# Performance work log

Hardware: AMD Instinct MI355X
Metric: run time of the kernel (lower is better)

## Reference

```python
import jax, jax.numpy as jnp
import numpy as np
import math

B, S, D, H = 2, 2048, 512, 8
HD = D // H

def setup_inputs() -> dict:
    key = jax.random.key(0)
    ks = jax.random.split(key, 13)
    scale = 1.0 / math.sqrt(D)
    inp = {
        "q_in": jax.random.normal(ks[0], (B, S, D), jnp.float32),
        "k_in": jax.random.normal(ks[1], (B, S, D), jnp.float32),
        "v_in": jax.random.normal(ks[2], (B, S, D), jnp.float32),
        "mask": jax.random.randint(ks[3], (B, 1, S, S), 0, 2, jnp.int32),
        "W1": jax.random.uniform(ks[4], (D, D), jnp.float32, -scale, scale),
        "b1": jax.random.uniform(ks[5], (D,), jnp.float32, -scale, scale),
        "W2": jax.random.uniform(ks[6], (D, D), jnp.float32, -scale, scale),
        "b2": jax.random.uniform(ks[7], (D,), jnp.float32, -scale, scale),
        "W3": jax.random.uniform(ks[8], (D, D), jnp.float32, -scale, scale),
        "b3": jax.random.uniform(ks[9], (D,), jnp.float32, -scale, scale),
        "Wo": jax.random.uniform(ks[10], (D, D), jnp.float32, -scale, scale),
        "bo": jax.random.uniform(ks[11], (D,), jnp.float32, -scale, scale),
    }
    return inp

def reference(q_in, k_in, v_in, mask, W1, b1, W2, b2, W3, b3, Wo, bo):
    # Linear projections (torch Linear: y = x @ W.T + b)
    q = q_in @ W1.T + b1  # [B,S,D]
    k = k_in @ W2.T + b2
    v = v_in @ W3.T + b3
    # split heads -> [B,H,S,HD]
    def split(x):
        return x.reshape(B, S, H, HD).transpose(0, 2, 1, 3)
    q, k, v = split(q), split(k), split(v)
    scores = jnp.einsum("bhqd,bhkd->bhqk", q, k) / math.sqrt(HD)
    scores = jnp.where(mask == 0, jnp.float32(-1e9), scores)
    attn = jax.nn.softmax(scores, axis=-1)
    out = jnp.einsum("bhqk,bhkd->bhqd", attn, v)  # [B,H,S,HD]
    out = out.transpose(0, 2, 1, 3).reshape(B, S, D)
    return out @ Wo.T + bo
```

## Files before the change

kernel.cpp:

```cpp
#include <hip/hip_runtime.h>
#include <hip/hip_bf16.h>
#include <math.h>

constexpr int B_ = 2, S_ = 2048, D_ = 512, H_ = 8, HD_ = 64;
constexpr int M_ = B_ * S_;
constexpr int NT_ = S_ / 64;
constexpr int NSPLIT = 2;
constexpr int NT2 = NT_ / NSPLIT;
constexpr int ROWS = B_ * S_ * H_;
constexpr int NGROUPS = (B_ * S_ * NT_) / 4;

typedef short s16x8 __attribute__((ext_vector_type(8)));
typedef float f32x4 __attribute__((ext_vector_type(4)));
typedef unsigned short u16;
typedef unsigned long long u64;

#define SWZ(b) ((b) ^ ((((b) >> 7) & 7) << 4))

constexpr float SCL = 0.18033688f;

static __device__ __forceinline__ unsigned int cvt_pk2(float lo, float hi) {
  __hip_bfloat162 h = __float22bfloat162_rn(make_float2(lo, hi));
  return *(unsigned int*)&h;
}
static __device__ __forceinline__ u16 cvt1(float f) {
  __hip_bfloat16 h = __float2bfloat16(f);
  return *(u16*)&h;
}
static __device__ __forceinline__ uint4 pack8(float4 a, float4 b) {
  uint4 r;
  r.x = cvt_pk2(a.x, a.y); r.y = cvt_pk2(a.z, a.w);
  r.z = cvt_pk2(b.x, b.y); r.w = cvt_pk2(b.z, b.w);
  return r;
}
static __device__ __forceinline__ float4 sum_scale(float4 a, float4 b, float s) {
  return make_float4((a.x + b.x) * s, (a.y + b.y) * s,
                     (a.z + b.z) * s, (a.w + b.w) * s);
}

#define QKV_STEP(BUF, T)                                                      \
  {                                                                           \
    const bool more_ = ((T) < 7);                                             \
    if (more_) {                                                              \
      const int o4 = ((T) + 1) * 16;                                          \
      fx[0] = Xb[o4];  fx[1] = Xb[o4 + 1];  fx[2] = Xb[o4 + 2];  fx[3] = Xb[o4 + 3]; \
      fw0[0] = W0b[o4]; fw0[1] = W0b[o4 + 1]; fw0[2] = W0b[o4 + 2]; fw0[3] = W0b[o4 + 3]; \
      fw1[0] = W1b[o4]; fw1[1] = W1b[o4 + 1]; fw1[2] = W1b[o4 + 2]; fw1[3] = W1b[o4 + 3]; \
    }                                                                         \
    __builtin_amdgcn_s_setprio(1);                                            \
    _Pragma("unroll")                                                         \
    for (int kw = 0; kw < 2; ++kw) {                                          \
      s16x8 af0 = *(const s16x8*)(shb + SWZ((BUF)*24576 + (wm*32 + l15)*128 + kw*64 + lg*16)); \
      s16x8 af1 = *(const s16x8*)(shb + SWZ((BUF)*24576 + (wm*32 + 16 + l15)*128 + kw*64 + lg*16)); \
      s16x8 b00 = *(const s16x8*)(shb + SWZ((BUF)*24576 + 8192 + (wn*32 + l15)*128 + kw*64 + lg*16)); \
      s16x8 b01 = *(const s16x8*)(shb + SWZ((BUF)*24576 + 8192 + (wn*32 + 16 + l15)*128 + kw*64 + lg*16)); \
      s16x8 b10 = *(const s16x8*)(shb + SWZ((BUF)*24576 + 16384 + (wn*32 + l15)*128 + kw*64 + lg*16)); \
      s16x8 b11 = *(const s16x8*)(shb + SWZ((BUF)*24576 + 16384 + (wn*32 + 16 + l15)*128 + kw*64 + lg*16)); \
      acc[0][0][0] = __builtin_amdgcn_mfma_f32_16x16x32_bf16(af0, b00, acc[0][0][0], 0, 0, 0); \
      acc[0][0][1] = __builtin_amdgcn_mfma_f32_16x16x32_bf16(af0, b01, acc[0][0][1], 0, 0, 0); \
      acc[0][1][0] = __builtin_amdgcn_mfma_f32_16x16x32_bf16(af1, b00, acc[0][1][0], 0, 0, 0); \
      acc[0][1][1] = __builtin_amdgcn_mfma_f32_16x16x32_bf16(af1, b01, acc[0][1][1], 0, 0, 0); \
      acc[1][0][0] = __builtin_amdgcn_mfma_f32_16x16x32_bf16(af0, b10, acc[1][0][0], 0, 0, 0); \
      acc[1][0][1] = __builtin_amdgcn_mfma_f32_16x16x32_bf16(af0, b11, acc[1][0][1], 0, 0, 0); \
      acc[1][1][0] = __builtin_amdgcn_mfma_f32_16x16x32_bf16(af1, b10, acc[1][1][0], 0, 0, 0); \
      acc[1][1][1] = __builtin_amdgcn_mfma_f32_16x16x32_bf16(af1, b11, acc[1][1][1], 0, 0, 0); \
    }                                                                         \
    __builtin_amdgcn_s_setprio(0);                                            \
    if (more_) {                                                              \
      char* p_ = shb + ((BUF) ^ 1) * 24576;                                   \
      *(uint4*)(p_ + SWZ(awb)) = pack8(fx[0], fx[1]);                         \
      *(uint4*)(p_ + SWZ(awb + 16)) = pack8(fx[2], fx[3]);                    \
      *(uint4*)(p_ + SWZ(b0wb)) = pack8(fw0[0], fw0[1]);                      \
      *(uint4*)(p_ + SWZ(b0wb + 16)) = pack8(fw0[2], fw0[3]);                 \
      *(uint4*)(p_ + SWZ(b1wb)) = pack8(fw1[0], fw1[1]);                      \
      *(uint4*)(p_ + SWZ(b1wb + 16)) = pack8(fw1[2], fw1[3]);                 \
    }                                                                         \
    __syncthreads();                                                          \
  }

__global__ __launch_bounds__(256) void gemm_qkv(
    const float* __restrict__ Xq, const float* __restrict__ Wq,
    const float* __restrict__ bq, u16* __restrict__ Yq,
    const float* __restrict__ Xk, const float* __restrict__ Wk,
    const float* __restrict__ bk, u16* __restrict__ Yk,
    const float* __restrict__ Xv, const float* __restrict__ Wv,
    const float* __restrict__ bv, u16* __restrict__ Yv,
    const int* __restrict__ mask, u64* __restrict__ mbits)
{
  const float* X; const float* W; const float* bias; u16* Y;
  const int z = blockIdx.z;
  if (z == 0)      { X = Xq; W = Wq; bias = bq; Y = Yq; }
  else if (z == 1) { X = Xk; W = Wk; bias = bk; Y = Yk; }
  else             { X = Xv; W = Wv; bias = bv; Y = Yv; }

  __shared__ __align__(128) char SH[2][24576];
  char* shb = &SH[0][0];

  const int tid = threadIdx.x;
  const int lane = tid & 63, w = tid >> 6;
  const int l15 = lane & 15, lg = lane >> 4;
  const int wm = w >> 1, wn = w & 1;
  const int m0 = blockIdx.x * 64, n0 = blockIdx.y * 128;
  const int sr = tid >> 2, sc = (tid & 3) * 16;

  const float4* Xb  = (const float4*)&X[(size_t)(m0 + sr) * D_ + sc];
  const float4* W0b = (const float4*)&W[(size_t)(n0 + sr) * D_ + sc];
  const float4* W1b = (const float4*)&W[(size_t)(n0 + 64 + sr) * D_ + sc];
  const int awb  = sr * 128 + (tid & 3) * 32;
  const int b0wb = 8192 + awb;
  const int b1wb = 16384 + awb;

  float4 fx[4], fw0[4], fw1[4];
#pragma unroll
  for (int i = 0; i < 4; ++i) { fx[i] = Xb[i]; fw0[i] = W0b[i]; fw1[i] = W1b[i]; }

  const int bid = blockIdx.x + blockIdx.y * gridDim.x +
                  blockIdx.z * gridDim.x * gridDim.y;
  const int gw = bid * 4 + w;
  int4 mv[10];
#pragma unroll
  for (int i = 0; i < 10; ++i)
    mv[i] = *(const int4*)&mask[(size_t)(gw + i * 3072) * 256 + lane * 4];
  const bool has10 = (gw + 10 * 3072) < NGROUPS;
  int4 mv10 = make_int4(0, 0, 0, 0);
  if (has10)
    mv10 = *(const int4*)&mask[(size_t)(gw + 10 * 3072) * 256 + lane * 4];
  __builtin_amdgcn_sched_barrier(0);

  f32x4 acc[2][2][2];
#pragma unroll
  for (int nh = 0; nh < 2; ++nh)
#pragma unroll
    for (int i = 0; i < 2; ++i)
#pragma unroll
      for (int j = 0; j < 2; ++j) acc[nh][i][j] = (f32x4){0.f, 0.f, 0.f, 0.f};

  {
    char* p = shb;
    *(uint4*)(p + SWZ(awb)) = pack8(fx[0], fx[1]);
    *(uint4*)(p + SWZ(awb + 16)) = pack8(fx[2], fx[3]);
    *(uint4*)(p + SWZ(b0wb)) = pack8(fw0[0], fw0[1]);
    *(uint4*)(p + SWZ(b0wb + 16)) = pack8(fw0[2], fw0[3]);
    *(uint4*)(p + SWZ(b1wb)) = pack8(fw1[0], fw1[1]);
    *(uint4*)(p + SWZ(b1wb + 16)) = pack8(fw1[2], fw1[3]);
  }
  __syncthreads();

#pragma unroll 1
  for (int tt = 0; tt < 8; tt += 2) {
    QKV_STEP(0, tt)
    QKV_STEP(1, tt + 1)
  }

  const float oscale = (z == 0) ? SCL : 1.0f;

  if (z != 2) {
#pragma unroll
    for (int nh = 0; nh < 2; ++nh) {
      float bias_v[2];
      bias_v[0] = bias[n0 + nh * 64 + wn * 32 + l15];
      bias_v[1] = bias[n0 + nh * 64 + wn * 32 + 16 + l15];
#pragma unroll
      for (int am = 0; am < 2; ++am)
#pragma unroll
        for (int bn = 0; bn < 2; ++bn)
#pragma unroll
          for (int j = 0; j < 4; ++j) {
            const int row = m0 + wm * 32 + am * 16 + lg * 4 + j;
            const int col = n0 + nh * 64 + wn * 32 + bn * 16 + l15;
            Y[(size_t)row * D_ + col] = cvt1((acc[nh][am][bn][j] + bias_v[bn]) * oscale);
          }
    }
  } else {
    const int batch = m0 >> 11, sb = m0 & (S_ - 1);
#pragma unroll
    for (int nh = 0; nh < 2; ++nh) {
      const int hh = blockIdx.y * 2 + nh;
      float bias_v[2];
      bias_v[0] = bias[n0 + nh * 64 + wn * 32 + l15];
      bias_v[1] = bias[n0 + nh * 64 + wn * 32 + 16 + l15];
      __syncthreads();
#pragma unroll
      for (int am = 0; am < 2; ++am)
#pragma unroll
        for (int bn = 0; bn < 2; ++bn) {
          const int dd = wn * 32 + bn * 16 + l15;
          const int sl = wm * 32 + am * 16 + lg * 4;
          ushort4 pk;
          pk.x = cvt1(acc[nh][am][bn][0] + bias_v[bn]);
          pk.y = cvt1(acc[nh][am][bn][1] + bias_v[bn]);
          pk.z = cvt1(acc[nh][am][bn][2] + bias_v[bn]);
          pk.w = cvt1(acc[nh][am][bn][3] + bias_v[bn]);
          *(ushort4*)(shb + SWZ(dd * 128 + sl * 2)) = pk;
        }
      __syncthreads();
      const int cr = sr * 128 + (tid & 3) * 32;
      uint4 c0 = *(uint4*)(shb + SWZ(cr));
      uint4 c1 = *(uint4*)(shb + SWZ(cr + 16));
      u16* dst = &Y[(((size_t)batch * H_ + hh) * 64 + sr) * S_ + sb + sc];
      *(uint4*)dst = c0;
      *(uint4*)(dst + 8) = c1;
    }
  }

#pragma unroll
  for (int i = 0; i < 10; ++i) {
    const int g = gw + i * 3072;
    u64 b0 = __ballot(mv[i].x != 0);
    u64 b1 = __ballot(mv[i].y != 0);
    u64 b2 = __ballot(mv[i].z != 0);
    u64 b3 = __ballot(mv[i].w != 0);
    if (lane < 4) {
      const int q = lane;
      u64 r = ((b0 >> (16 * q)) & 0xFFFFULL)
            | (((b1 >> (16 * q)) & 0xFFFFULL) << 16)
            | (((b2 >> (16 * q)) & 0xFFFFULL) << 32)
            | (((b3 >> (16 * q)) & 0xFFFFULL) << 48);
      mbits[(size_t)g * 4 + q] = r;
    }
  }
  {
    u64 b0 = __ballot(mv10.x != 0);
    u64 b1 = __ballot(mv10.y != 0);
    u64 b2 = __ballot(mv10.z != 0);
    u64 b3 = __ballot(mv10.w != 0);
    if (has10 && lane < 4) {
      const int g = gw + 10 * 3072;
      const int q = lane;
      u64 r = ((b0 >> (16 * q)) & 0xFFFFULL)
            | (((b1 >> (16 * q)) & 0xFFFFULL) << 16)
            | (((b2 >> (16 * q)) & 0xFFFFULL) << 32)
            | (((b3 >> (16 * q)) & 0xFFFFULL) << 48);
      mbits[(size_t)g * 4 + q] = r;
    }
  }
}

#define OPROJ_STEP(BUF, T)                                                    \
  {                                                                           \
    const bool more_ = ((T) < 7);                                             \
    if (more_) {                                                              \
      const int t1 = (T) + 1;                                                 \
      const float4* q0 = (const float4*)(poR + t1 * 64);                      \
      const float4* q1 = (const float4*)(poR + 2097152 + t1 * 64);            \
      float4 s0 = q0[0], s1 = q0[1], s2 = q0[2], s3 = q0[3];                  \
      float4 u0 = q1[0], u1 = q1[1], u2 = q1[2], u3 = q1[3];                  \
      const float li = 1.0f / (plR[t1] + plR[ROWS + t1]);                     \
      ax[0] = pack8(sum_scale(s0, u0, li), sum_scale(s1, u1, li));            \
      ax[1] = pack8(sum_scale(s2, u2, li), sum_scale(s3, u3, li));            \
      const int o4 = t1 * 16;                                                 \
      fw[0] = Wb[o4]; fw[1] = Wb[o4 + 1]; fw[2] = Wb[o4 + 2]; fw[3] = Wb[o4 + 3]; \
    }                                                                         \
    __builtin_amdgcn_s_setprio(1);                                            \
    _Pragma("unroll")                                                         \
    for (int kw = 0; kw < 2; ++kw) {                                          \
      s16x8 af0 = *(const s16x8*)(shb + SWZ((BUF)*16384 + (wm*32 + l15)*128 + kw*64 + lg*16)); \
      s16x8 af1 = *(const s16x8*)(shb + SWZ((BUF)*16384 + (wm*32 + 16 + l15)*128 + kw*64 + lg*16)); \
      s16x8 bf0 = *(const s16x8*)(shb + SWZ((BUF)*16384 + 8192 + (wn*32 + l15)*128 + kw*64 + lg*16)); \
      s16x8 bf1 = *(const s16x8*)(shb + SWZ((BUF)*16384 + 8192 + (wn*32 + 16 + l15)*128 + kw*64 + lg*16)); \
      acc[0][0] = __builtin_amdgcn_mfma_f32_16x16x32_bf16(af0, bf0, acc[0][0], 0, 0, 0); \
      acc[0][1] = __builtin_amdgcn_mfma_f32_16x16x32_bf16(af0, bf1, acc[0][1], 0, 0, 0); \
      acc[1][0] = __builtin_amdgcn_mfma_f32_16x16x32_bf16(af1, bf0, acc[1][0], 0, 0, 0); \
      acc[1][1] = __builtin_amdgcn_mfma_f32_16x16x32_bf16(af1, bf1, acc[1][1], 0, 0, 0); \
    }                                                                         \
    __builtin_amdgcn_s_setprio(0);                                            \
    if (more_) {                                                              \
      char* p_ = shb + ((BUF) ^ 1) * 16384;                                   \
      *(uint4*)(p_ + SWZ(awb)) = ax[0];                                       \
      *(uint4*)(p_ + SWZ(awb + 16)) = ax[1];                                  \
      *(uint4*)(p_ + SWZ(bwb)) = pack8(fw[0], fw[1]);                         \
      *(uint4*)(p_ + SWZ(bwb + 16)) = pack8(fw[2], fw[3]);                    \
    }                                                                         \
    __syncthreads();                                                          \
  }

__global__ __launch_bounds__(256) void gemm_oproj(
    const float* __restrict__ po, const float* __restrict__ pl,
    const float* __restrict__ W, const float* __restrict__ bias,
    float* __restrict__ Y)
{
  __shared__ __align__(128) u16 SH[2][2][64][64];
  char* shb = (char*)SH;

  const int tid = threadIdx.x;
  const int lane = tid & 63, w = tid >> 6;
  const int l15 = lane & 15, lg = lane >> 4;
  const int wm = w >> 1, wn = w & 1;
  const int m0 = blockIdx.x * 64, n0 = blockIdx.y * 64;
  const int sr = tid >> 2, sc = (tid & 3) * 16;

  const float* poR = po + (size_t)(m0 + sr) * 512 + sc;
  const float* plR = pl + (size_t)(m0 + sr) * 8;
  const float4* Wb = (const float4*)&W[(size_t)(n0 + sr) * D_ + sc];
  const int awb = sr * 128 + (tid & 3) * 32;
  const int bwb = 8192 + sr * 128 + (tid & 3) * 32;

  f32x4 acc[2][2];
#pragma unroll
  for (int i = 0; i < 2; ++i)
#pragma unroll
    for (int j = 0; j < 2; ++j) acc[i][j] = (f32x4){0.f, 0.f, 0.f, 0.f};

  uint4 ax[2]; float4 fw[4];
  {
    const float4* q0 = (const float4*)(poR);
    const float4* q1 = (const float4*)(poR + 2097152);
    float4 s0 = q0[0], s1 = q0[1], s2 = q0[2], s3 = q0[3];
    float4 u0 = q1[0], u1 = q1[1], u2 = q1[2], u3 = q1[3];
    const float li = 1.0f / (plR[0] + plR[ROWS]);
    ax[0] = pack8(sum_scale(s0, u0, li), sum_scale(s1, u1, li));
    ax[1] = pack8(sum_scale(s2, u2, li), sum_scale(s3, u3, li));
#pragma unroll
    for (int i = 0; i < 4; ++i) fw[i] = Wb[i];
    char* p = shb;
    *(uint4*)(p + SWZ(awb)) = ax[0];
    *(uint4*)(p + SWZ(awb + 16)) = ax[1];
    *(uint4*)(p + SWZ(bwb)) = pack8(fw[0], fw[1]);
    *(uint4*)(p + SWZ(bwb + 16)) = pack8(fw[2], fw[3]);
  }
  __syncthreads();

#pragma unroll 1
  for (int tt = 0; tt < 8; tt += 2) {
    OPROJ_STEP(0, tt)
    OPROJ_STEP(1, tt + 1)
  }

  float bias_v[2];
  bias_v[0] = bias[n0 + wn * 32 + l15];
  bias_v[1] = bias[n0 + wn * 32 + 16 + l15];
#pragma unroll
  for (int am = 0; am < 2; ++am)
#pragma unroll
    for (int bn = 0; bn < 2; ++bn)
#pragma unroll
      for (int j = 0; j < 4; ++j) {
        const int row = m0 + wm * 32 + am * 16 + lg * 4 + j;
        const int col = n0 + wn * 32 + bn * 16 + l15;
        Y[(size_t)row * D_ + col] = acc[am][bn][j] + bias_v[bn];
      }
}

__global__ __launch_bounds__(256) void attn_mfma(
    const u16* __restrict__ qp, const u16* __restrict__ kp,
    const u16* __restrict__ vt, const u64* __restrict__ mbits,
    float* __restrict__ po, float* __restrict__ pl)
{
  const int fid = blockIdx.x + 32 * (blockIdx.y + 8 * blockIdx.z);
  const int d = (fid & 7) * 128 + (fid >> 3);
  const int bx = d & 31, by = (d >> 5) & 7, bz = d >> 8;

  const int b = bz >> 1, half = bz & 1;
  const int h = by;
  const int q0 = bx * 64;
  const int kt0 = half * (S_ / NSPLIT);
  const int tid = threadIdx.x;
  const int lane = tid & 63;
  const int w = tid >> 6;
  const int l15 = lane & 15, lg = lane >> 4;

  __shared__ __align__(128) u16 KV[2][2][64][64];
  __shared__ __align__(128) u16 Pl[4][16][64];
  char* kvb = (char*)KV;
  char* plb = (char*)Pl;

  const int qr = q0 + w * 16;

  const u16* qrow = qp + ((size_t)b * S_ + qr + l15) * D_ + h * HD_;
  const s16x8 qf0 = *(const s16x8*)(qrow + lg * 8);
  const s16x8 qf1 = *(const s16x8*)(qrow + 32 + lg * 8);

  s16x8 onesf;
#pragma unroll
  for (int i = 0; i < 8; ++i) onesf[i] = (short)0x3F80;

  f32x4 out[4];
#pragma unroll
  for (int dt = 0; dt < 4; ++dt) out[dt] = (f32x4){0.f, 0.f, 0.f, 0.f};
  float l_s = 0.f;

  const int sr = tid >> 2;
  const int sc = (tid & 3) * 16;
  const u16* kbase = kp + (size_t)b * S_ * D_ + h * HD_;
  const u16* vbase = vt + (((size_t)b * H_ + h) * 64 + sr) * (size_t)S_ + kt0 + sc;
  const u64* mrow = mbits + ((size_t)b * S_ + qr + l15) * NT_ + half * NT2;

  const int mX = (l15 & 7) << 4;
  const int rd_lo = ((l15 << 7) + lg * 16) ^ mX;
  const int rd_hi = rd_lo ^ 64;
  const int mW = (sr & 7) << 4;
  const int wr_lo = ((sr << 7) + (tid & 3) * 32) ^ mW;
  const int wr_hi = wr_lo ^ 16;
  const int pq = w * 2048 + l15 * 128;
  const int pw0 = (pq + lg * 8) ^ mX;
  const int pa_lo = (pq + lg * 16) ^ mX;
  const int pa_hi = pa_lo ^ 64;

  uint4 rk0, rk1, rv0, rv1;
  {
    const u16* ksrc = kbase + (size_t)(kt0 + sr) * D_ + sc;
    rk0 = *(const uint4*)ksrc; rk1 = *(const uint4*)(ksrc + 8);
    rv0 = *(const uint4*)vbase; rv1 = *(const uint4*)(vbase + 8);
    *(uint4*)(kvb + wr_lo) = rk0;
    *(uint4*)(kvb + wr_hi) = rk1;
    *(uint4*)(kvb + wr_lo + 8192) = rv0;
    *(uint4*)(kvb + wr_hi + 8192) = rv1;
  }
  u64 msk = mrow[0];
  __syncthreads();

#pragma unroll 1
  for (int t = 0; t < NT2; ++t) {
    const int cur = t & 1;
    const bool more = (t + 1 < NT2);
    u64 msk_n = 0;
    if (more) {
      const int kt = (t + 1) * 64;
      const u16* ksrc = kbase + (size_t)(kt0 + kt + sr) * D_ + sc;
      rk0 = *(const uint4*)ksrc; rk1 = *(const uint4*)(ksrc + 8);
      rv0 = *(const uint4*)(vbase + kt); rv1 = *(const uint4*)(vbase + kt + 8);
      msk_n = mrow[t + 1];
    }

    const unsigned mlo = (unsigned)(msk >> lg);
    const unsigned mhi = (unsigned)(msk >> (lg + 32));

    char* rb_lo = kvb + (cur << 14) + rd_lo;
    char* rb_hi = kvb + (cur << 14) + rd_hi;

    f32x4 z[4];
    __builtin_amdgcn_s_setprio(1);
#pragma unroll
    for (int t4 = 0; t4 < 4; ++t4) {
      s16x8 kb0 = *(const s16x8*)(rb_lo + t4 * 2048);
      s16x8 kb1 = *(const s16x8*)(rb_hi + t4 * 2048);
      f32x4 zz = (f32x4){0.f, 0.f, 0.f, 0.f};
      zz = __builtin_amdgcn_mfma_f32_16x16x32_bf16(kb0, qf0, zz, 0, 0, 0);
      zz = __builtin_amdgcn_mfma_f32_16x16x32_bf16(kb1, qf1, zz, 0, 0, 0);
      z[t4] = zz;
    }
    __builtin_amdgcn_s_setprio(0);

    float x[4][4];
#pragma unroll
    for (int t4 = 0; t4 < 4; ++t4) {
#pragma unroll
      for (int r = 0; r < 4; ++r) {
        const unsigned bit = (r < 2) ? ((mlo >> (16 * r + 4 * t4)) & 1u)
                                     : ((mhi >> (16 * (r - 2) + 4 * t4)) & 1u);
        float xv = bit ? z[t4][r] : -1.0e9f;
        x[t4][r] = exp2f(xv);
      }
    }

#pragma unroll
    for (int t4 = 0; t4 < 4; ++t4) {
      uint2 pk;
      pk.x = cvt_pk2(x[t4][0], x[t4][1]);
      pk.y = cvt_pk2(x[t4][2], x[t4][3]);
      *(uint2*)(plb + (pw0 ^ (t4 * 32))) = pk;
    }

    s16x8 pa0 = *(const s16x8*)(plb + pa_lo);
    s16x8 pa1 = *(const s16x8*)(plb + pa_hi);

    __builtin_amdgcn_s_setprio(1);
    f32x4 zl = (f32x4){0.f, 0.f, 0.f, 0.f};
    zl = __builtin_amdgcn_mfma_f32_16x16x32_bf16(onesf, pa0, zl, 0, 0, 0);
    zl = __builtin_amdgcn_mfma_f32_16x16x32_bf16(onesf, pa1, zl, 0, 0, 0);
#pragma unroll
    for (int dt = 0; dt < 4; ++dt) {
      s16x8 va0 = *(const s16x8*)(rb_lo + 8192 + dt * 2048);
      s16x8 va1 = *(const s16x8*)(rb_hi + 8192 + dt * 2048);
      out[dt] = __builtin_amdgcn_mfma_f32_16x16x32_bf16(va0, pa0, out[dt], 0, 0, 0);
      out[dt] = __builtin_amdgcn_mfma_f32_16x16x32_bf16(va1, pa1, out[dt], 0, 0, 0);
    }
    __builtin_amdgcn_s_setprio(0);
    l_s += zl[0];

    if (more) {
      char* wb_lo = kvb + ((cur ^ 1) << 14) + wr_lo;
      char* wb_hi = kvb + ((cur ^ 1) << 14) + wr_hi;
      *(uint4*)(wb_lo) = rk0;
      *(uint4*)(wb_hi) = rk1;
      *(uint4*)(wb_lo + 8192) = rv0;
      *(uint4*)(wb_hi + 8192) = rv1;
      msk = msk_n;
    }
    __syncthreads();
  }

  const int rowi = ((b * S_ + qr + l15) * H_) + h;
  float* pobase = po + ((size_t)half * ROWS + rowi) * 64;
#pragma unroll
  for (int dt = 0; dt < 4; ++dt) {
    float4 o = make_float4(out[dt][0], out[dt][1], out[dt][2], out[dt][3]);
    *(float4*)&pobase[dt * 16 + lg * 4] = o;
  }
  if (lg == 0) pl[(size_t)half * ROWS + rowi] = l_s;
}

extern "C" void kernel_launch(void* const* d_in, const int* in_sizes, int n_in,
                              void* d_out, int out_size, void* d_ws,
                              size_t ws_size, hipStream_t stream)
{
  const float* q_in = (const float*)d_in[0];
  const float* k_in = (const float*)d_in[1];
  const float* v_in = (const float*)d_in[2];
  const int*   mask = (const int*)d_in[3];
  const float* W1 = (const float*)d_in[4];
  const float* b1 = (const float*)d_in[5];
  const float* W2 = (const float*)d_in[6];
  const float* b2 = (const float*)d_in[7];
  const float* W3 = (const float*)d_in[8];
  const float* b3 = (const float*)d_in[9];
  const float* Wo = (const float*)d_in[10];
  const float* bo = (const float*)d_in[11];
  float* out = (float*)d_out;

  char* ws = (char*)d_ws;
  u16* qp = (u16*)ws;
  u16* kp = (u16*)(ws + (4u << 20));
  u16* vtp = (u16*)(ws + (8u << 20));
  u64* mbits = (u64*)(ws + (12u << 20));
  float* pl = (float*)(ws + (13u << 20));
  float* po = (float*)(ws + (13u << 20) + (512u << 10));

  dim3 blk(256);
  gemm_qkv<<<dim3(M_ / 64, D_ / 128, 3), blk, 0, stream>>>(
      q_in, W1, b1, qp, k_in, W2, b2, kp, v_in, W3, b3, vtp, mask, mbits);
  attn_mfma<<<dim3(S_ / 64, H_, B_ * NSPLIT), blk, 0, stream>>>(
      qp, kp, vtp, mbits, po, pl);
  gemm_oproj<<<dim3(M_ / 64, D_ / 64), blk, 0, stream>>>(po, pl, Wo, bo, out);
}
```

Baseline: 90.18 us.

## Double attention query tile to 128 rows with 512-thread blocks sharing K/V tiles

The attention kernel now processes 128 query rows per block using 8 waves instead of 64 rows with 4 waves, so each K/V tile staged in shared memory is reused by twice as many queries. Global-to-LDS staging is redistributed so each of the 512 threads loads one 16-byte chunk of K and of V instead of two. The launch grid halves in x and the block-id swizzle is adjusted to match. This cuts redundant K/V global traffic but halves the block count (to 512 blocks) and raises per-block register and LDS pressure, which may reduce occupancy.

```diff
diff --git a/kernel.cpp b/kernel.cpp
--- a/kernel.cpp
+++ b/kernel.cpp
@@ -341,18 +341,18 @@
       }
 }
 
-__global__ __launch_bounds__(256) void attn_mfma(
+__global__ __launch_bounds__(512) void attn_mfma(
     const u16* __restrict__ qp, const u16* __restrict__ kp,
     const u16* __restrict__ vt, const u64* __restrict__ mbits,
     float* __restrict__ po, float* __restrict__ pl)
 {
-  const int fid = blockIdx.x + 32 * (blockIdx.y + 8 * blockIdx.z);
-  const int d = (fid & 7) * 128 + (fid >> 3);
-  const int bx = d & 31, by = (d >> 5) & 7, bz = d >> 8;
+  const int fid = blockIdx.x + 16 * (blockIdx.y + 8 * blockIdx.z);
+  const int d = (fid & 7) * 64 + (fid >> 3);
+  const int bx = d & 15, by = (d >> 4) & 7, bz = d >> 7;
 
   const int b = bz >> 1, half = bz & 1;
   const int h = by;
-  const int q0 = bx * 64;
+  const int q0 = bx * 128;
   const int kt0 = half * (S_ / NSPLIT);
   const int tid = threadIdx.x;
   const int lane = tid & 63;
@@ -360,7 +360,7 @@
   const int l15 = lane & 15, lg = lane >> 4;
 
   __shared__ __align__(128) u16 KV[2][2][64][64];
-  __shared__ __align__(128) u16 Pl[4][16][64];
+  __shared__ __align__(128) u16 Pl[8][16][64];
   char* kvb = (char*)KV;
   char* plb = (char*)Pl;
 
@@ -379,32 +379,28 @@
   for (int dt = 0; dt < 4; ++dt) out[dt] = (f32x4){0.f, 0.f, 0.f, 0.f};
   float l_s = 0.f;
 
-  const int sr = tid >> 2;
-  const int sc = (tid & 3) * 16;
+  const int sr8 = tid >> 3;
+  const int sc8 = (tid & 7) * 8;
   const u16* kbase = kp + (size_t)b * S_ * D_ + h * HD_;
-  const u16* vbase = vt + (((size_t)b * H_ + h) * 64 + sr) * (size_t)S_ + kt0 + sc;
+  const u16* vbase = vt + (((size_t)b * H_ + h) * 64 + sr8) * (size_t)S_ + kt0 + sc8;
   const u64* mrow = mbits + ((size_t)b * S_ + qr + l15) * NT_ + half * NT2;
 
   const int mX = (l15 & 7) << 4;
   const int rd_lo = ((l15 << 7) + lg * 16) ^ mX;
   const int rd_hi = rd_lo ^ 64;
-  const int mW = (sr & 7) << 4;
-  const int wr_lo = ((sr << 7) + (tid & 3) * 32) ^ mW;
-  const int wr_hi = wr_lo ^ 16;
+  const int wr_k = ((sr8 << 7) + (tid & 7) * 16) ^ ((sr8 & 7) << 4);
   const int pq = w * 2048 + l15 * 128;
   const int pw0 = (pq + lg * 8) ^ mX;
   const int pa_lo = (pq + lg * 16) ^ mX;
   const int pa_hi = pa_lo ^ 64;
 
-  uint4 rk0, rk1, rv0, rv1;
+  uint4 rk0, rv0;
   {
-    const u16* ksrc = kbase + (size_t)(kt0 + sr) * D_ + sc;
-    rk0 = *(const uint4*)ksrc; rk1 = *(const uint4*)(ksrc + 8);
-    rv0 = *(const uint4*)vbase; rv1 = *(const uint4*)(vbase + 8);
-    *(uint4*)(kvb + wr_lo) = rk0;
-    *(uint4*)(kvb + wr_hi) = rk1;
-    *(uint4*)(kvb + wr_lo + 8192) = rv0;
-    *(uint4*)(kvb + wr_hi + 8192) = rv1;
+    const u16* ksrc = kbase + (size_t)(kt0 + sr8) * D_ + sc8;
+    rk0 = *(const uint4*)ksrc;
+    rv0 = *(const uint4*)vbase;
+    *(uint4*)(kvb + wr_k) = rk0;
+    *(uint4*)(kvb + wr_k + 8192) = rv0;
   }
   u64 msk = mrow[0];
   __syncthreads();
@@ -416,9 +412,8 @@
     u64 msk_n = 0;
     if (more) {
       const int kt = (t + 1) * 64;
-      const u16* ksrc = kbase + (size_t)(kt0 + kt + sr) * D_ + sc;
-      rk0 = *(const uint4*)ksrc; rk1 = *(const uint4*)(ksrc + 8);
-      rv0 = *(const uint4*)(vbase + kt); rv1 = *(const uint4*)(vbase + kt + 8);
+      rk0 = *(const uint4*)(kbase + (size_t)(kt0 + kt + sr8) * D_ + sc8);
+      rv0 = *(const uint4*)(vbase + kt);
       msk_n = mrow[t + 1];
     }
 
@@ -479,12 +474,9 @@
     l_s += zl[0];
 
     if (more) {
-      char* wb_lo = kvb + ((cur ^ 1) << 14) + wr_lo;
-      char* wb_hi = kvb + ((cur ^ 1) << 14) + wr_hi;
-      *(uint4*)(wb_lo) = rk0;
-      *(uint4*)(wb_hi) = rk1;
-      *(uint4*)(wb_lo + 8192) = rv0;
-      *(uint4*)(wb_hi + 8192) = rv1;
+      char* wb = kvb + ((cur ^ 1) << 14) + wr_k;
+      *(uint4*)(wb) = rk0;
+      *(uint4*)(wb + 8192) = rv0;
       msk = msk_n;
     }
     __syncthreads();
@@ -526,10 +518,9 @@
   float* pl = (float*)(ws + (13u << 20));
   float* po = (float*)(ws + (13u << 20) + (512u << 10));
 
-  dim3 blk(256);
-  gemm_qkv<<<dim3(M_ / 64, D_ / 128, 3), blk, 0, stream>>>(
+  gemm_qkv<<<dim3(M_ / 64, D_ / 128, 3), dim3(256), 0, stream>>>(
       q_in, W1, b1, qp, k_in, W2, b2, kp, v_in, W3, b3, vtp, mask, mbits);
-  attn_mfma<<<dim3(S_ / 64, H_, B_ * NSPLIT), blk, 0, stream>>>(
+  attn_mfma<<<dim3(S_ / 128, H_, B_ * NSPLIT), dim3(512), 0, stream>>>(
       qp, kp, vtp, mbits, po, pl);
-  gemm_oproj<<<dim3(M_ / 64, D_ / 64), blk, 0, stream>>>(po, pl, Wo, bo, out);
-}
+  gemm_oproj<<<dim3(M_ / 64, D_ / 64), dim3(256), 0, stream>>>(po, pl, Wo, bo, out);
+}
```

Result: no change. 90.34 us (+0.2%).
